# Kernel tuning notes

Measured on AMD Instinct MI355X. Metric: run time of the kernel, lower is better.

## Reference

```python
import jax, jax.numpy as jnp
import numpy as np

B = 128
J = 22
Q = J * 4          # 88
R = 3
C = 4
H = 512            # LSTM hidden
ENC = 256 * 3      # 768 concatenated encoder outputs
STATE_IN = Q + R + C   # 95
OFF_IN = Q + R         # 91
OUT = Q + R + C        # 95


def _linear_params(key, fan_in, fan_out):
    kw, kb = jax.random.split(key)
    s = 1.0 / np.sqrt(fan_in)
    w = jax.random.uniform(kw, (fan_in, fan_out), jnp.float32, -s, s)
    b = jax.random.uniform(kb, (fan_out,), jnp.float32, -s, s)
    return w, b


def setup_inputs() -> dict:
    key = jax.random.key(0)
    ks = jax.random.split(key, 24)
    inp = {
        "past_root_vel": jax.random.normal(ks[0], (B, 10, R)) * 0.1,
        "past_quats": jax.random.normal(ks[1], (B, 10, Q)),
        "past_root_offset": jax.random.normal(ks[2], (B, 10, R)),
        "past_quat_offset": jax.random.normal(ks[3], (B, 10, Q)),
        "past_contacts": jax.random.uniform(ks[4], (B, 10, C)),
        "target_root_pos": jax.random.normal(ks[5], (B, R)),
        "target_quats": jax.random.normal(ks[6], (B, Q)),
        "init_root_pos": jax.random.normal(ks[7], (B, R)),
        "pred_weights": jax.random.normal(ks[8], (B, 4 * H, ENC + H)) * 0.03,
        "pred_bias": jax.random.normal(ks[9], (B, 4 * H)) * 0.01,
    }
    inp["se_w1"], inp["se_b1"] = _linear_params(ks[10], STATE_IN, 512)
    inp["se_w2"], inp["se_b2"] = _linear_params(ks[11], 512, 256)
    inp["oe_w1"], inp["oe_b1"] = _linear_params(ks[12], OFF_IN, 512)
    inp["oe_w2"], inp["oe_b2"] = _linear_params(ks[13], 512, 256)
    inp["te_w1"], inp["te_b1"] = _linear_params(ks[14], Q, 512)
    inp["te_w2"], inp["te_b2"] = _linear_params(ks[15], 512, 256)
    inp["de_w1"], inp["de_b1"] = _linear_params(ks[16], H, 512)
    inp["de_w2"], inp["de_b2"] = _linear_params(ks[17], 512, 256)
    inp["de_w3"], inp["de_b3"] = _linear_params(ks[18], 256, OUT)
    return inp


def reference(past_root_vel, past_quats, past_root_offset, past_quat_offset,
              past_contacts, target_root_pos, target_quats, init_root_pos,
              pred_weights, pred_bias,
              se_w1, se_b1, se_w2, se_b2,
              oe_w1, oe_b1, oe_w2, oe_b2,
              te_w1, te_b1, te_w2, te_b2,
              de_w1, de_b1, de_w2, de_b2, de_w3, de_b3):
    b = past_quats.shape[0]

    def enc(x, w1, b1, w2, b2):
        return jax.nn.relu(jax.nn.relu(x @ w1 + b1) @ w2 + b2)

    # target encoding is identical every step; hoist it
    h_target = enc(target_quats, te_w1, te_b1, te_w2, te_b2)

    def step(root_vel, quats, root_offset, quat_offset, contacts, h, c):
        state_vec = jnp.concatenate([contacts, quats, root_vel], axis=1)
        offset_vec = jnp.concatenate([root_offset, quat_offset], axis=1)
        h_state = enc(state_vec, se_w1, se_b1, se_w2, se_b2)
        h_offset = enc(offset_vec, oe_w1, oe_b1, oe_w2, oe_b2)
        pred_in = jnp.concatenate([h_state, h_offset, h_target], axis=1)  # [B,768]
        # per-sample hypernetwork LSTM cell (torch gate order i,f,g,o)
        z = jnp.concatenate([pred_in, h], axis=1)  # [B, 1280]
        gates = jnp.einsum('boi,bi->bo', pred_weights, z) + pred_bias
        i_g, f_g, g_g, o_g = jnp.split(gates, 4, axis=1)
        c2 = jax.nn.sigmoid(f_g) * c + jax.nn.sigmoid(i_g) * jnp.tanh(g_g)
        h2 = jax.nn.sigmoid(o_g) * jnp.tanh(c2)
        # decoder (512,512,256,out), no activation on last layer
        d = jax.nn.relu(h2 @ de_w1 + de_b1)
        d = jax.nn.relu(d @ de_w2 + de_b2)
        out = d @ de_w3 + de_b3
        next_quats = out[:, :Q] + quats
        next_rvel = out[:, Q:Q + R] + root_vel
        next_contacts = jax.nn.sigmoid(out[:, Q + R:])
        nq = next_quats.reshape(b, Q // 4, 4)
        nq = nq / jnp.maximum(jnp.linalg.norm(nq, axis=2, keepdims=True), 1e-12)
        return next_rvel, nq.reshape(b, Q), next_contacts, h2, c2

    h0 = jnp.zeros((b, H), past_quats.dtype)
    c0 = jnp.zeros((b, H), past_quats.dtype)

    def past_body(carry, x):
        glob, h, c, _, _, _, _, _ = carry
        rvel, quats, roff, qoff, cont = x
        nrv, nq, nc, h2, c2 = step(rvel, quats, roff, qoff, cont, h, c)
        glob2 = glob + rvel
        nroff = glob2 - target_root_pos
        nqoff = nq - target_quats
        return (glob2, h2, c2, nrv, nq, nc, nroff, nqoff), None

    z3 = jnp.zeros((b, R), past_quats.dtype)
    init = (init_root_pos, h0, c0, z3,
            jnp.zeros((b, Q), past_quats.dtype),
            jnp.zeros((b, C), past_quats.dtype),
            z3, jnp.zeros((b, Q), past_quats.dtype))
    xs = (jnp.swapaxes(past_root_vel, 0, 1), jnp.swapaxes(past_quats, 0, 1),
          jnp.swapaxes(past_root_offset, 0, 1), jnp.swapaxes(past_quat_offset, 0, 1),
          jnp.swapaxes(past_contacts, 0, 1))
    carry, _ = jax.lax.scan(past_body, init, xs)
    glob, h, c, nrv, nq, nc, roff, qoff = carry

    first_frame = jnp.concatenate([nrv, nq], axis=1)  # NOTE: rvel not glob, as in source

    def trans_body(carry, _):
        glob, h, c, rvel, quats, cont, roff, qoff = carry
        nrv, nq, nc, h2, c2 = step(rvel, quats, roff, qoff, cont, h, c)
        glob2 = glob + nrv
        nroff = glob2 - target_root_pos
        nqoff = nq - target_quats
        pose = jnp.concatenate([glob2, nq], axis=1)
        return (glob2, h2, c2, nrv, nq, nc, nroff, nqoff), (pose, nc)

    carry2 = (glob, h, c, nrv, nq, nc, roff, qoff)
    _, (poses, conts) = jax.lax.scan(trans_body, carry2, None, length=29)

    pred_poses = jnp.concatenate([first_frame[:, None], jnp.swapaxes(poses, 0, 1)], axis=1)
    pred_contacts = jnp.concatenate([nc[:, None], jnp.swapaxes(conts, 0, 1)], axis=1)
    return pred_poses, pred_contacts
```

## Files before the change

### kernel.cpp

```cpp
#include <hip/hip_runtime.h>
#include <hip/hip_bf16.h>
#include <math.h>

#define BATCH 128
#define QD 88
#define HDIM 512
#define ZDIM 1280
#define GDIM 2048
#define PROW 1536
#define NPAST 10
#define NTRANS 29
#define NSTEPS (NPAST + NTRANS)
#define OUTD 95
#define POSE_ELEMS (BATCH * 30 * 91)

typedef float f32x4 __attribute__((ext_vector_type(4)));

__device__ __forceinline__ float sig_(float x) { return 1.0f / (1.0f + expf(-x)); }
__device__ __forceinline__ void dot4_(const uint4 wv, const float4 zv, float& d) {
    const float4 f = *(const float4*)&wv;
    d = fmaf(f.x, zv.x, d); d = fmaf(f.y, zv.y, d);
    d = fmaf(f.z, zv.z, d); d = fmaf(f.w, zv.w, d);
}
__device__ __forceinline__ void fma4_(float4& acc, float x, const float4 w) {
    acc.x = fmaf(x, w.x, acc.x); acc.y = fmaf(x, w.y, acc.y);
    acc.z = fmaf(x, w.z, acc.z); acc.w = fmaf(x, w.w, acc.w);
}
__device__ __forceinline__ unsigned q12_(float w, float inv) {
    const unsigned u = __float2uint_rn(fmaf(w, inv, 2048.0f));
    return (u > 4095u) ? 4095u : u;
}
__device__ __forceinline__ void pack12_(const uint4 a, const uint4 b, float inv,
                                        unsigned& o0, unsigned& o1, unsigned& o2) {
    const unsigned u0 = q12_(__uint_as_float(a.x), inv), u1 = q12_(__uint_as_float(a.y), inv);
    const unsigned u2 = q12_(__uint_as_float(a.z), inv), u3 = q12_(__uint_as_float(a.w), inv);
    const unsigned u4 = q12_(__uint_as_float(b.x), inv), u5 = q12_(__uint_as_float(b.y), inv);
    const unsigned u6 = q12_(__uint_as_float(b.z), inv), u7 = q12_(__uint_as_float(b.w), inv);
    o0 = u0 | (u1 << 12) | (u2 << 24);
    o1 = (u2 >> 8) | (u3 << 4) | (u4 << 16) | (u5 << 28);
    o2 = (u5 >> 4) | (u6 << 8) | (u7 << 20);
}
__device__ __forceinline__ float dot12_(unsigned d0, unsigned d1, unsigned d2,
                                        const float4 za, const float4 zb) {
    float acc = 0.f;
    acc = fmaf((float)((int)(d0 & 0xFFFu) - 2048), za.x, acc);
    acc = fmaf((float)((int)((d0 >> 12) & 0xFFFu) - 2048), za.y, acc);
    acc = fmaf((float)((int)((d0 >> 24) | ((d1 & 0xFu) << 8)) - 2048), za.z, acc);
    acc = fmaf((float)((int)((d1 >> 4) & 0xFFFu) - 2048), za.w, acc);
    acc = fmaf((float)((int)((d1 >> 16) & 0xFFFu) - 2048), zb.x, acc);
    acc = fmaf((float)((int)((d1 >> 28) | ((d2 & 0xFFu) << 4)) - 2048), zb.y, acc);
    acc = fmaf((float)((int)((d2 >> 8) & 0xFFFu) - 2048), zb.z, acc);
    acc = fmaf((float)((int)(d2 >> 20) - 2048), zb.w, acc);
    return acc;
}
__device__ __forceinline__ float wredmax_(float m) {
    #pragma unroll
    for (int s = 32; s >= 1; s >>= 1) m = fmaxf(m, __shfl_xor(m, s, 64));
    return m;
}
__device__ __forceinline__ float amax4_(const uint4 a, float m) {
    m = fmaxf(m, fabsf(__uint_as_float(a.x))); m = fmaxf(m, fabsf(__uint_as_float(a.y)));
    m = fmaxf(m, fabsf(__uint_as_float(a.z))); m = fmaxf(m, fabsf(__uint_as_float(a.w)));
    return m;
}

__global__ void __launch_bounds__(256)
matvec0_conv(const float* __restrict__ W, const float* __restrict__ z_ws,
             const float* __restrict__ pred_bias, unsigned char* __restrict__ Wp,
             float* __restrict__ scale_ws, float* __restrict__ g_ws, float* __restrict__ g0_ws)
{
    const int b = blockIdx.x >> 5, chunk = blockIdx.x & 31;
    const int wave = threadIdx.x >> 6, lane = threadIdx.x & 63;
    const int row0 = chunk * 64 + wave * 16;
    const float* zb = z_ws + b * ZDIM;
    const float biasv = (lane < 16) ? pred_bias[b * GDIM + row0 + lane] : 0.f;
    const int l4 = lane * 4;
    const float4 z0 = *(const float4*)(zb + l4);
    const float4 z1 = *(const float4*)(zb + 256 + l4);
    const float4 zh = *(const float4*)(zb + 512 + l4);
    const float4 z3 = *(const float4*)(zb + 768 + l4);
    const float4 z4 = *(const float4*)(zb + 1024 + l4);
    const char* wb = (const char*)W + (size_t)b * GDIM * ZDIM * 4;
    char* dstB = (char*)Wp + (size_t)b * GDIM * PROW;

    #define ISSUE(p, B) { const char* a_ = wb + (size_t)(row0 + 2 * (p)) * (ZDIM * 4) + lane * 16; \
        _Pragma("unroll") for (int i = 0; i < 10; ++i) B[i] = *(const uint4*)(a_ + i * 1024); }

    uint4 bufa[10], bufb[10];
    ISSUE(0, bufa);
    #pragma unroll
    for (int p = 0; p < 8; ++p) {
        uint4* cur = (p & 1) ? bufb : bufa;
        uint4* nxt = (p & 1) ? bufa : bufb;
        if (p < 7) ISSUE(p + 1, nxt);
        float dynA = 0.f, dynB = 0.f, statA = 0.f, statB = 0.f;
        dot4_(cur[0], z0, dynA); dot4_(cur[1], z1, dynA);
        dot4_(cur[2], zh, statA);
        dot4_(cur[3], z3, dynA); dot4_(cur[4], z4, dynA);
        dot4_(cur[5], z0, dynB); dot4_(cur[6], z1, dynB);
        dot4_(cur[7], zh, statB);
        dot4_(cur[8], z3, dynB); dot4_(cur[9], z4, dynB);
        float m0 = 0.f, m1 = 0.f;
        m0 = amax4_(cur[0], m0); m0 = amax4_(cur[1], m0);
        m0 = amax4_(cur[3], m0); m0 = amax4_(cur[4], m0);
        m1 = amax4_(cur[5], m1); m1 = amax4_(cur[6], m1);
        m1 = amax4_(cur[8], m1); m1 = amax4_(cur[9], m1);
        m0 = wredmax_(m0); m1 = wredmax_(m1);
        const float s0 = m0 * (1.f / 2047.f), s1 = m1 * (1.f / 2047.f);
        const float inv0 = (m0 > 0.f) ? 2047.f / m0 : 0.f;
        const float inv1 = (m1 > 0.f) ? 2047.f / m1 : 0.f;
        {
            char* rp = dstB + (size_t)(row0 + 2 * p) * PROW + lane * 12;
            unsigned o0, o1, o2;
            pack12_(cur[0], cur[1], inv0, o0, o1, o2);
            __builtin_nontemporal_store(o0, (unsigned*)(rp));
            __builtin_nontemporal_store(o1, (unsigned*)(rp + 4));
            __builtin_nontemporal_store(o2, (unsigned*)(rp + 8));
            pack12_(cur[3], cur[4], inv0, o0, o1, o2);
            __builtin_nontemporal_store(o0, (unsigned*)(rp + 768));
            __builtin_nontemporal_store(o1, (unsigned*)(rp + 772));
            __builtin_nontemporal_store(o2, (unsigned*)(rp + 776));
            pack12_(cur[5], cur[6], inv1, o0, o1, o2);
            __builtin_nontemporal_store(o0, (unsigned*)(rp + 1536));
            __builtin_nontemporal_store(o1, (unsigned*)(rp + 1540));
            __builtin_nontemporal_store(o2, (unsigned*)(rp + 1544));
            pack12_(cur[8], cur[9], inv1, o0, o1, o2);
            __builtin_nontemporal_store(o0, (unsigned*)(rp + 2304));
            __builtin_nontemporal_store(o1, (unsigned*)(rp + 2308));
            __builtin_nontemporal_store(o2, (unsigned*)(rp + 2312));
        }
        if (lane == 0) { scale_ws[b * GDIM + row0 + 2 * p] = s0;
                         scale_ws[b * GDIM + row0 + 2 * p + 1] = s1; }
        float sd0 = dynA + __shfl_xor(dynA, 32);
        float sd1 = dynB + __shfl_xor(dynB, 32);
        float ud = (lane < 32) ? sd0 : sd1;
        float ss0 = statA + __shfl_xor(statA, 32);
        float ss1 = statB + __shfl_xor(statB, 32);
        float us = (lane < 32) ? ss0 : ss1;
        #pragma unroll
        for (int m = 16; m >= 1; m >>= 1) { ud += __shfl_xor(ud, m); us += __shfl_xor(us, m); }
        const float badd = __shfl(biasv, 2 * p + ((lane >= 32) ? 1 : 0), 64);
        if (lane == 0 || lane == 32) {
            const int r = row0 + 2 * p + ((lane >= 32) ? 1 : 0);
            g0_ws[b * GDIM + r] = us + badd;
            g_ws[b * GDIM + r]  = ud + us + badd;
        }
    }
    #undef ISSUE
}

__global__ void __launch_bounds__(256)
epass(const unsigned char* __restrict__ Wp, const float* __restrict__ enc9,
      const float* __restrict__ scale_ws, const float* __restrict__ g0_ws,
      float* __restrict__ E_ws)
{
    const int b = blockIdx.x >> 5, chunk = blockIdx.x & 31;
    const int wave = threadIdx.x >> 6, lane = threadIdx.x & 63;
    const int row0 = chunk * 64 + wave * 16;
    const int l4 = lane * 4;
    float4 eA[9], eB[9];
    #pragma unroll
    for (int s = 0; s < 9; ++s) {
        const float* eb = enc9 + ((size_t)s * BATCH + b) * 512;
        eA[s] = *(const float4*)(eb + l4);
        eB[s] = *(const float4*)(eb + 256 + l4);
    }
    const float g0v = (lane < 16) ? g0_ws[b * GDIM + row0 + lane] : 0.f;
    const float scv = (lane < 16) ? scale_ws[b * GDIM + row0 + lane] : 0.f;
    const char* wb = (const char*)Wp + (size_t)b * GDIM * PROW;

    #define ISSUE(p, B) { const char* a_ = wb + (size_t)(row0 + 2 * (p)) * PROW + lane * 12; \
        B[0] = __builtin_nontemporal_load((const unsigned*)(a_)); \
        B[1] = __builtin_nontemporal_load((const unsigned*)(a_ + 4)); \
        B[2] = __builtin_nontemporal_load((const unsigned*)(a_ + 8)); \
        B[3] = __builtin_nontemporal_load((const unsigned*)(a_ + 1536)); \
        B[4] = __builtin_nontemporal_load((const unsigned*)(a_ + 1540)); \
        B[5] = __builtin_nontemporal_load((const unsigned*)(a_ + 1544)); }

    unsigned bufa[6], bufb[6];
    ISSUE(0, bufa);
    #pragma unroll
    for (int p = 0; p < 8; ++p) {
        unsigned* cur = (p & 1) ? bufb : bufa;
        unsigned* nxt = (p & 1) ? bufa : bufb;
        if (p < 7) ISSUE(p + 1, nxt);
        const float badd = __shfl(g0v, 2 * p + ((lane >= 32) ? 1 : 0), 64);
        const float srow = __shfl(scv, 2 * p + ((lane >= 32) ? 1 : 0), 64);
        #pragma unroll
        for (int s = 0; s < 9; ++s) {
            const float aA = dot12_(cur[0], cur[1], cur[2], eA[s], eB[s]);
            const float aB = dot12_(cur[3], cur[4], cur[5], eA[s], eB[s]);
            const float s0 = aA + __shfl_xor(aA, 32);
            const float s1 = aB + __shfl_xor(aB, 32);
            float u = (lane < 32) ? s0 : s1;
            #pragma unroll
            for (int m = 16; m >= 1; m >>= 1) u += __shfl_xor(u, m);
            const float val = badd + srow * u;
            if (lane == 0)
                E_ws[((size_t)s * BATCH + b) * GDIM + row0 + 2 * p] = val;
            else if (lane == 32)
                E_ws[((size_t)s * BATCH + b) * GDIM + row0 + 2 * p + 1] = val;
        }
    }
    #undef ISSUE
}

__global__ void __launch_bounds__(256)
matvecH(const unsigned char* __restrict__ Wp, const float* __restrict__ z_ws,
        const float* __restrict__ scale_ws, const float* __restrict__ Es,
        float* __restrict__ g_ws)
{
    const int b = blockIdx.x >> 5, chunk = blockIdx.x & 31;
    const int wave = threadIdx.x >> 6, lane = threadIdx.x & 63;
    const int row0 = chunk * 64 + wave * 16;
    const float* zb = z_ws + b * ZDIM;
    const int l4 = lane * 4;
    const float4 z3 = *(const float4*)(zb + 768 + l4);
    const float4 z4 = *(const float4*)(zb + 1024 + l4);
    const float Ev  = (lane < 16) ? Es[b * GDIM + row0 + lane] : 0.f;
    const float scv = (lane < 16) ? scale_ws[b * GDIM + row0 + lane] : 0.f;
    const char* wb = (const char*)Wp + (size_t)b * GDIM * PROW;

    #define ISSUE(p, B) { const char* a_ = wb + (size_t)(row0 + 2 * (p)) * PROW + 768 + lane * 12; \
        B[0] = *(const unsigned*)(a_);        B[1] = *(const unsigned*)(a_ + 4); \
        B[2] = *(const unsigned*)(a_ + 8); \
        B[3] = *(const unsigned*)(a_ + 1536); B[4] = *(const unsigned*)(a_ + 1540); \
        B[5] = *(const unsigned*)(a_ + 1544); }

    unsigned buf0[6], buf1[6], buf2[6];
    ISSUE(0, buf0);
    ISSUE(1, buf1);
    #pragma unroll
    for (int p = 0; p < 8; ++p) {
        unsigned* cur = (p % 3 == 0) ? buf0 : (p % 3 == 1) ? buf1 : buf2;
        unsigned* nxt = ((p + 2) % 3 == 0) ? buf0 : ((p + 2) % 3 == 1) ? buf1 : buf2;
        if (p < 6) ISSUE(p + 2, nxt);
        const float aA = dot12_(cur[0], cur[1], cur[2], z3, z4);
        const float aB = dot12_(cur[3], cur[4], cur[5], z3, z4);
        const float s0 = aA + __shfl_xor(aA, 32);
        const float s1 = aB + __shfl_xor(aB, 32);
        float u = (lane < 32) ? s0 : s1;
        #pragma unroll
        for (int m = 16; m >= 1; m >>= 1) u += __shfl_xor(u, m);
        const float badd = __shfl(Ev, 2 * p + ((lane >= 32) ? 1 : 0), 64);
        const float srow = __shfl(scv, 2 * p + ((lane >= 32) ? 1 : 0), 64);
        const float val = badd + srow * u;
        if (lane == 0)       g_ws[b * GDIM + row0 + 2 * p]     = val;
        else if (lane == 32) g_ws[b * GDIM + row0 + 2 * p + 1] = val;
    }
    #undef ISSUE
}

__global__ void __launch_bounds__(256)
matvec12(const unsigned char* __restrict__ Wp, const float* __restrict__ z_ws,
         const float* __restrict__ scale_ws, const float* __restrict__ g0_ws,
         float* __restrict__ g_ws)
{
    const int b = blockIdx.x >> 5, chunk = blockIdx.x & 31;
    const int wave = threadIdx.x >> 6, lane = threadIdx.x & 63;
    const int row0 = chunk * 64 + wave * 16;
    const float* zb = z_ws + b * ZDIM;
    const int l4 = lane * 4;
    const float4 z0 = *(const float4*)(zb + l4);
    const float4 z1 = *(const float4*)(zb + 256 + l4);
    const float4 z3 = *(const float4*)(zb + 768 + l4);
    const float4 z4 = *(const float4*)(zb + 1024 + l4);
    const float g0v = (lane < 16) ? g0_ws[b * GDIM + row0 + lane] : 0.f;
    const float scv = (lane < 16) ? scale_ws[b * GDIM + row0 + lane] : 0.f;
    const char* wb = (const char*)Wp + (size_t)b * GDIM * PROW;

    #define ISSUE(p, B) { const char* a_ = wb + (size_t)(row0 + 2 * (p)) * PROW + lane * 12; \
        B[0] = __builtin_nontemporal_load((const unsigned*)(a_)); \
        B[1] = __builtin_nontemporal_load((const unsigned*)(a_ + 4)); \
        B[2] = __builtin_nontemporal_load((const unsigned*)(a_ + 8)); \
        B[3] = __builtin_nontemporal_load((const unsigned*)(a_ + 768)); \
        B[4] = __builtin_nontemporal_load((const unsigned*)(a_ + 772)); \
        B[5] = __builtin_nontemporal_load((const unsigned*)(a_ + 776)); \
        B[6] = __builtin_nontemporal_load((const unsigned*)(a_ + 1536)); \
        B[7] = __builtin_nontemporal_load((const unsigned*)(a_ + 1540)); \
        B[8] = __builtin_nontemporal_load((const unsigned*)(a_ + 1544)); \
        B[9] = __builtin_nontemporal_load((const unsigned*)(a_ + 2304)); \
        B[10] = __builtin_nontemporal_load((const unsigned*)(a_ + 2308)); \
        B[11] = __builtin_nontemporal_load((const unsigned*)(a_ + 2312)); }

    unsigned buf0[12], buf1[12], buf2[12];
    ISSUE(0, buf0);
    ISSUE(1, buf1);
    #pragma unroll
    for (int p = 0; p < 8; ++p) {
        unsigned* cur = (p % 3 == 0) ? buf0 : (p % 3 == 1) ? buf1 : buf2;
        unsigned* nxt = ((p + 2) % 3 == 0) ? buf0 : ((p + 2) % 3 == 1) ? buf1 : buf2;
        if (p < 6) ISSUE(p + 2, nxt);
        const float aA = dot12_(cur[0], cur[1], cur[2], z0, z1)
                       + dot12_(cur[3], cur[4], cur[5], z3, z4);
        const float aB = dot12_(cur[6], cur[7], cur[8], z0, z1)
                       + dot12_(cur[9], cur[10], cur[11], z3, z4);
        const float s0 = aA + __shfl_xor(aA, 32);
        const float s1 = aB + __shfl_xor(aB, 32);
        float u = (lane < 32) ? s0 : s1;
        #pragma unroll
        for (int m = 16; m >= 1; m >>= 1) u += __shfl_xor(u, m);
        const float badd = __shfl(g0v, 2 * p + ((lane >= 32) ? 1 : 0), 64);
        const float srow = __shfl(scv, 2 * p + ((lane >= 32) ? 1 : 0), 64);
        const float val = badd + srow * u;
        if (lane == 0)       g_ws[b * GDIM + row0 + 2 * p]     = val;
        else if (lane == 32) g_ws[b * GDIM + row0 + 2 * p + 1] = val;
    }
    #undef ISSUE
}

__global__ void __launch_bounds__(512)
initk(const float* __restrict__ past_root_vel, const float* __restrict__ past_quats,
      const float* __restrict__ past_root_offset, const float* __restrict__ past_quat_offset,
      const float* __restrict__ past_contacts, const float* __restrict__ target_quats,
      const float* __restrict__ init_root_pos,
      const float* __restrict__ se_w1, const float* __restrict__ se_b1,
      const float* __restrict__ se_w2, const float* __restrict__ se_b2,
      const float* __restrict__ oe_w1, const float* __restrict__ oe_b1,
      const float* __restrict__ oe_w2, const float* __restrict__ oe_b2,
      const float* __restrict__ te_w1, const float* __restrict__ te_b1,
      const float* __restrict__ te_w2, const float* __restrict__ te_b2,
      float* __restrict__ z_ws, float* __restrict__ c_ws, float* __restrict__ car_ws)
{
    const int b = blockIdx.x, t = threadIdx.x;
    __shared__ float tq[QD], bufA[512], bufB[512], sv[95], ov[91];

    if (t < 192) car_ws[b * 192 + t] = (t < 3) ? init_root_pos[b * 3 + t] : 0.f;
    c_ws[b * HDIM + t] = 0.f;
    z_ws[b * ZDIM + 768 + t] = 0.f;
    if (t < QD) tq[t] = target_quats[b * QD + t];
    if (t < 4)  sv[t] = past_contacts[b * NPAST * 4 + t];
    if (t < QD) { sv[4 + t] = past_quats[b * NPAST * QD + t];
                  ov[3 + t] = past_quat_offset[b * NPAST * QD + t]; }
    if (t < 3)  { sv[92 + t] = past_root_vel[b * NPAST * 3 + t];
                  ov[t]      = past_root_offset[b * NPAST * 3 + t]; }
    __syncthreads();
    {
        float a = te_b1[t];
        #pragma unroll 8
        for (int i = 0; i < QD; ++i) a = fmaf(tq[i], te_w1[i * 512 + t], a);
        bufA[t] = fmaxf(a, 0.f);
    }
    __syncthreads();
    if (t < 256) {
        float a = te_b2[t];
        #pragma unroll 8
        for (int i = 0; i < 512; ++i) a = fmaf(bufA[i], te_w2[i * 256 + t], a);
        z_ws[b * ZDIM + 512 + t] = fmaxf(a, 0.f);
    }
    __syncthreads();
    {
        float aS = se_b1[t], aO = oe_b1[t];
        #pragma unroll 8
        for (int i = 0; i < 91; ++i) { aS = fmaf(sv[i], se_w1[i * 512 + t], aS);
                                       aO = fmaf(ov[i], oe_w1[i * 512 + t], aO); }
        #pragma unroll
        for (int i = 91; i < 95; ++i) aS = fmaf(sv[i], se_w1[i * 512 + t], aS);
        bufA[t] = fmaxf(aS, 0.f);
        bufB[t] = fmaxf(aO, 0.f);
    }
    __syncthreads();
    if (t < 256) {
        float a = se_b2[t];
        #pragma unroll 8
        for (int i = 0; i < 512; ++i) a = fmaf(bufA[i], se_w2[i * 256 + t], a);
        z_ws[b * ZDIM + t] = fmaxf(a, 0.f);
    } else {
        const int j = t - 256;
        float a = oe_b2[j];
        #pragma unroll 8
        for (int i = 0; i < 512; ++i) a = fmaf(bufB[i], oe_w2[i * 256 + j], a);
        z_ws[b * ZDIM + 256 + j] = fmaxf(a, 0.f);
    }
}

__global__ void __launch_bounds__(512)
enc_past(const float* __restrict__ past_root_vel, const float* __restrict__ past_quats,
         const float* __restrict__ past_root_offset, const float* __restrict__ past_quat_offset,
         const float* __restrict__ past_contacts,
         const float* __restrict__ se_w1, const float* __restrict__ se_b1,
         const float* __restrict__ se_w2, const float* __restrict__ se_b2,
         const float* __restrict__ oe_w1, const float* __restrict__ oe_b1,
         const float* __restrict__ oe_w2, const float* __restrict__ oe_b2,
         float* __restrict__ enc9)
{
    const int b = blockIdx.x, t = threadIdx.x;
    const int s = blockIdx.y + 1;
    __shared__ float bufA[512], bufB[512], sv[95], ov[91];

    if (t < 4)  sv[t] = past_contacts[(b * NPAST + s) * 4 + t];
    if (t < QD) { sv[4 + t] = past_quats[(b * NPAST + s) * QD + t];
                  ov[3 + t] = past_quat_offset[(b * NPAST + s) * QD + t]; }
    if (t < 3)  { sv[92 + t] = past_root_vel[(b * NPAST + s) * 3 + t];
                  ov[t]      = past_root_offset[(b * NPAST + s) * 3 + t]; }
    __syncthreads();
    {
        float aS = se_b1[t], aO = oe_b1[t];
        #pragma unroll 8
        for (int i = 0; i < 91; ++i) { aS = fmaf(sv[i], se_w1[i * 512 + t], aS);
                                       aO = fmaf(ov[i], oe_w1[i * 512 + t], aO); }
        #pragma unroll
        for (int i = 91; i < 95; ++i) aS = fmaf(sv[i], se_w1[i * 512 + t], aS);
        bufA[t] = fmaxf(aS, 0.f);
        bufB[t] = fmaxf(aO, 0.f);
    }
    __syncthreads();
    float* dst = enc9 + ((size_t)(s - 1) * BATCH + b) * 512;
    if (t < 256) {
        float a = se_b2[t];
        #pragma unroll 8
        for (int i = 0; i < 512; ++i) a = fmaf(bufA[i], se_w2[i * 256 + t], a);
        dst[t] = fmaxf(a, 0.f);
    } else {
        const int j = t - 256;
        float a = oe_b2[j];
        #pragma unroll 8
        for (int i = 0; i < 512; ++i) a = fmaf(bufB[i], oe_w2[i * 256 + j], a);
        dst[256 + j] = fmaxf(a, 0.f);
    }
}

__global__ void __launch_bounds__(512)
stepk(const float* __restrict__ past_root_vel, const float* __restrict__ past_quats,
      const float* __restrict__ past_root_offset, const float* __restrict__ past_quat_offset,
      const float* __restrict__ past_contacts, const float* __restrict__ target_root_pos,
      const float* __restrict__ target_quats,
      const float* __restrict__ se_w1, const float* __restrict__ se_b1,
      const float* __restrict__ se_w2, const float* __restrict__ se_b2,
      const float* __restrict__ oe_w1, const float* __restrict__ oe_b1,
      const float* __restrict__ oe_w2, const float* __restrict__ oe_b2,
      const float* __restrict__ de_w1, const float* __restrict__ de_b1,
      const float* __restrict__ de_w2, const float* __restrict__ de_b2,
      const float* __restrict__ de_w3, const float* __restrict__ de_b3,
      float* __restrict__ out, float* __restrict__ z_ws, const float* __restrict__ g_ws,
      float* __restrict__ c_ws, float* __restrict__ car_ws, int s, int skip_enc)
{
    const int b = blockIdx.x, t = threadIdx.x;
    __shared__ float4 part4[512];
    __shared__ __align__(16) float h2s[HDIM], bufA[512], bufB[512], d2[256];
    __shared__ float outv[OUTD], nq[QD], sv[95], ov[91], carryL[192], tq[QD], trp[3];
    __shared__ float rvn[3], globn[3], contn[4];

    if (t < 192) carryL[t] = car_ws[b * 192 + t];
    if (t < QD) tq[t] = target_quats[b * QD + t];
    if (t < 3)  trp[t] = target_root_pos[b * 3 + t];

    {
        const float* g = g_ws + b * GDIM;
        const float ig = g[t], fg = g[512 + t], gg = g[1024 + t], og = g[1536 + t];
        const float c2 = sig_(fg) * c_ws[b * HDIM + t] + sig_(ig) * tanhf(gg);
        c_ws[b * HDIM + t] = c2;
        const float h2 = sig_(og) * tanhf(c2);
        h2s[t] = h2;
        z_ws[b * ZDIM + 768 + t] = h2;
    }
    __syncthreads();
    {
        const int c = t & 127, s4 = t >> 7;
        float4 acc = {0.f, 0.f, 0.f, 0.f};
        const float* w = de_w1 + (size_t)(s4 * 128) * 512 + 4 * c;
        #pragma unroll 8
        for (int k = 0; k < 128; ++k)
            fma4_(acc, h2s[s4 * 128 + k], *(const float4*)(w + (size_t)k * 512));
        part4[t] = acc;
    }
    __syncthreads();
    if (t < 128) {
        float4 v = part4[t];
        #pragma unroll
        for (int s4 = 1; s4 < 4; ++s4) { const float4 p = part4[s4 * 128 + t];
            v.x += p.x; v.y += p.y; v.z += p.z; v.w += p.w; }
        const float4 bb = *(const float4*)(de_b1 + 4 * t);
        float4 r; r.x = fmaxf(v.x + bb.x, 0.f); r.y = fmaxf(v.y + bb.y, 0.f);
        r.z = fmaxf(v.z + bb.z, 0.f); r.w = fmaxf(v.w + bb.w, 0.f);
        *(float4*)&bufA[4 * t] = r;
    }
    __syncthreads();
    {
        const int c = t & 63, s8 = t >> 6;
        float4 acc = {0.f, 0.f, 0.f, 0.f};
        const float* w = de_w2 + (size_t)(s8 * 64) * 256 + 4 * c;
        #pragma unroll 8
        for (int k = 0; k < 64; ++k)
            fma4_(acc, bufA[s8 * 64 + k], *(const float4*)(w + (size_t)k * 256));
        part4[t] = acc;
    }
    __syncthreads();
    if (t < 64) {
        float4 v = part4[t];
        #pragma unroll
        for (int s8 = 1; s8 < 8; ++s8) { const float4 p = part4[s8 * 64 + t];
            v.x += p.x; v.y += p.y; v.z += p.z; v.w += p.w; }
        const float4 bb = *(const float4*)(de_b2 + 4 * t);
        float4 r; r.x = fmaxf(v.x + bb.x, 0.f); r.y = fmaxf(v.y + bb.y, 0.f);
        r.z = fmaxf(v.z + bb.z, 0.f); r.w = fmaxf(v.w + bb.w, 0.f);
        *(float4*)&d2[4 * t] = r;
    }
    __syncthreads();
    if (t < OUTD) {
        float acc = de_b3[t];
        #pragma unroll 16
        for (int i = 0; i < 256; ++i) acc = fmaf(d2[i], de_w3[i * OUTD + t], acc);
        outv[t] = acc;
    }
    __syncthreads();

    const bool pastS = (s < NPAST);
    if (t < QD) {
        const float qin = pastS ? past_quats[(b * NPAST + s) * QD + t] : carryL[10 + t];
        nq[t] = outv[t] + qin;
    }
    __syncthreads();
    if (t < 22) {
        const float a = nq[4 * t], b2 = nq[4 * t + 1], c3 = nq[4 * t + 2], d4 = nq[4 * t + 3];
        const float inv = 1.f / fmaxf(sqrtf(a * a + b2 * b2 + c3 * c3 + d4 * d4), 1e-12f);
        nq[4 * t] = a * inv; nq[4 * t + 1] = b2 * inv; nq[4 * t + 2] = c3 * inv; nq[4 * t + 3] = d4 * inv;
    }
    if (t < 3) {
        const float rin = pastS ? past_root_vel[(b * NPAST + s) * 3 + t] : carryL[3 + t];
        const float nrv = outv[88 + t] + rin;
        const float g = carryL[t] + (pastS ? rin : nrv);
        rvn[t] = nrv; globn[t] = g;
    }
    if (t < 4) contn[t] = sig_(outv[91 + t]);
    __syncthreads();

    if (t < 3) { car_ws[b * 192 + t] = globn[t]; car_ws[b * 192 + 3 + t] = rvn[t];
                 car_ws[b * 192 + 186 + t] = globn[t] - trp[t]; }
    if (t < 4) car_ws[b * 192 + 6 + t] = contn[t];
    if (t < QD) { car_ws[b * 192 + 10 + t] = nq[t]; car_ws[b * 192 + 98 + t] = nq[t] - tq[t]; }
    if (s == NPAST - 1) {
        const size_t pb = (size_t)b * 30 * 91;
        if (t < 3)  out[pb + t] = rvn[t];
        if (t < QD) out[pb + 3 + t] = nq[t];
        if (t < 4)  out[POSE_ELEMS + (size_t)b * 30 * 4 + t] = contn[t];
    } else if (!pastS) {
        const int k = s - NPAST + 1;
        const size_t pb = ((size_t)b * 30 + k) * 91;
        if (t < 3)  out[pb + t] = globn[t];
        if (t < QD) out[pb + 3 + t] = nq[t];
        if (t < 4)  out[POSE_ELEMS + ((size_t)b * 30 + k) * 4 + t] = contn[t];
    }
    if (s == NSTEPS - 1) return;
    if (skip_enc) return;

    const int nx = s + 1;
    if (nx < NPAST) {
        if (t < 4)  sv[t] = past_contacts[(b * NPAST + nx) * 4 + t];
        if (t < QD) { sv[4 + t] = past_quats[(b * NPAST + nx) * QD + t];
                      ov[3 + t] = past_quat_offset[(b * NPAST + nx) * QD + t]; }
        if (t < 3)  { sv[92 + t] = past_root_vel[(b * NPAST + nx) * 3 + t];
                      ov[t]      = past_root_offset[(b * NPAST + nx) * 3 + t]; }
    } else {
        if (t < 4)  sv[t] = contn[t];
        if (t < QD) { sv[4 + t] = nq[t]; ov[3 + t] = nq[t] - tq[t]; }
        if (t < 3)  { sv[92 + t] = rvn[t]; ov[t] = globn[t] - trp[t]; }
    }
    __syncthreads();
    {
        const int tt = t & 255, enc = t >> 8;
        const int c = tt & 127, sl = tt >> 7;
        const float* inp = enc ? ov : sv;
        const float* w1  = enc ? oe_w1 : se_w1;
        const int nin  = enc ? 91 : 95;
        const int half = enc ? 46 : 48;
        const int i0 = sl * half;
        const int iend = (i0 + half < nin) ? (i0 + half) : nin;
        float4 acc = {0.f, 0.f, 0.f, 0.f};
        #pragma unroll 8
        for (int k = 0; k < 48; ++k) {
            const int i = i0 + k;
            if (i < iend) fma4_(acc, inp[i], *(const float4*)(w1 + (size_t)i * 512 + 4 * c));
        }
        part4[enc * 256 + tt] = acc;
    }
    __syncthreads();
    if (t < 128) {
        const float4 a = part4[t], b2 = part4[128 + t];
        const float4 bb = *(const float4*)(se_b1 + 4 * t);
        float4 r; r.x = fmaxf(a.x + b2.x + bb.x, 0.f); r.y = fmaxf(a.y + b2.y + bb.y, 0.f);
        r.z = fmaxf(a.z + b2.z + bb.z, 0.f); r.w = fmaxf(a.w + b2.w + bb.w, 0.f);
        *(float4*)&bufA[4 * t] = r;
    } else if (t < 256) {
        const int c = t - 128;
        const float4 a = part4[256 + c], b2 = part4[384 + c];
        const float4 bb = *(const float4*)(oe_b1 + 4 * c);
        float4 r; r.x = fmaxf(a.x + b2.x + bb.x, 0.f); r.y = fmaxf(a.y + b2.y + bb.y, 0.f);
        r.z = fmaxf(a.z + b2.z + bb.z, 0.f); r.w = fmaxf(a.w + b2.w + bb.w, 0.f);
        *(float4*)&bufB[4 * c] = r;
    }
    __syncthreads();
    {
        const int tt = t & 255, enc = t >> 8;
        const int c = tt & 63, sl = tt >> 6;
        const float* inp = enc ? bufB : bufA;
        const float* w2  = enc ? oe_w2 : se_w2;
        float4 acc = {0.f, 0.f, 0.f, 0.f};
        const float* w = w2 + (size_t)(sl * 128) * 256 + 4 * c;
        #pragma unroll 8
        for (int k = 0; k < 128; ++k)
            fma4_(acc, inp[sl * 128 + k], *(const float4*)(w + (size_t)k * 256));
        part4[enc * 256 + tt] = acc;
    }
    __syncthreads();
    if (t < 64) {
        float4 v = part4[t];
        #pragma unroll
        for (int sl = 1; sl < 4; ++sl) { const float4 p = part4[sl * 64 + t];
            v.x += p.x; v.y += p.y; v.z += p.z; v.w += p.w; }
        const float4 bb = *(const float4*)(se_b2 + 4 * t);
        float4 r; r.x = fmaxf(v.x + bb.x, 0.f); r.y = fmaxf(v.y + bb.y, 0.f);
        r.z = fmaxf(v.z + bb.z, 0.f); r.w = fmaxf(v.w + bb.w, 0.f);
        *(float4*)(z_ws + b * ZDIM + 4 * t) = r;
    } else if (t < 128) {
        const int c = t - 64;
        float4 v = part4[256 + c];
        #pragma unroll
        for (int sl = 1; sl < 4; ++sl) { const float4 p = part4[256 + sl * 64 + c];
            v.x += p.x; v.y += p.y; v.z += p.z; v.w += p.w; }
        const float4 bb = *(const float4*)(oe_b2 + 4 * c);
        float4 r; r.x = fmaxf(v.x + bb.x, 0.f); r.y = fmaxf(v.y + bb.y, 0.f);
        r.z = fmaxf(v.z + bb.z, 0.f); r.w = fmaxf(v.w + bb.w, 0.f);
        *(float4*)(z_ws + b * ZDIM + 256 + 4 * c) = r;
    }
}

__global__ void __launch_bounds__(256)
matvec_f32(const float* __restrict__ W, const float* __restrict__ z_ws,
           const float* __restrict__ pred_bias, float* __restrict__ g_ws)
{
    const int b = blockIdx.x >> 5, chunk = blockIdx.x & 31;
    const int wave = threadIdx.x >> 6, lane = threadIdx.x & 63;
    const int row0 = chunk * 64 + wave * 16;
    const float* zb = z_ws + b * ZDIM;
    const float biasv = (lane < 16) ? pred_bias[b * GDIM + row0 + lane] : 0.f;
    const int l4 = lane * 4;
    const float4 z0 = *(const float4*)(zb + l4);
    const float4 z1 = *(const float4*)(zb + 256 + l4);
    const float4 z2 = *(const float4*)(zb + 512 + l4);
    const float4 z3 = *(const float4*)(zb + 768 + l4);
    const float4 z4 = *(const float4*)(zb + 1024 + l4);
    const char* wb = (const char*)W + (size_t)b * GDIM * ZDIM * 4;

    #define ISSUE(p, B) { const char* a_ = wb + (size_t)(row0 + 2 * (p)) * (ZDIM * 4) + lane * 16; \
        _Pragma("unroll") for (int i = 0; i < 10; ++i) B[i] = *(const uint4*)(a_ + i * 1024); }

    uint4 bufa[10], bufb[10];
    ISSUE(0, bufa);
    #pragma unroll
    for (int p = 0; p < 8; ++p) {
        uint4* cur = (p & 1) ? bufb : bufa;
        uint4* nxt = (p & 1) ? bufa : bufb;
        if (p < 7) ISSUE(p + 1, nxt);
        float accA = 0.f, accB = 0.f;
        dot4_(cur[0], z0, accA); dot4_(cur[1], z1, accA); dot4_(cur[2], z2, accA);
        dot4_(cur[3], z3, accA); dot4_(cur[4], z4, accA);
        dot4_(cur[5], z0, accB); dot4_(cur[6], z1, accB); dot4_(cur[7], z2, accB);
        dot4_(cur[8], z3, accB); dot4_(cur[9], z4, accB);
        float s0 = accA + __shfl_xor(accA, 32);
        float s1 = accB + __shfl_xor(accB, 32);
        float u = (lane < 32) ? s0 : s1;
        #pragma unroll
        for (int m = 16; m >= 1; m >>= 1) u += __shfl_xor(u, m);
        const float badd = __shfl(biasv, 2 * p + ((lane >= 32) ? 1 : 0), 64);
        if (lane == 0)       g_ws[b * GDIM + row0 + 2 * p]     = u + badd;
        else if (lane == 32) g_ws[b * GDIM + row0 + 2 * p + 1] = u + badd;
    }
    #undef ISSUE
}

extern "C" void kernel_launch(void* const* d_in, const int* in_sizes, int n_in,
                              void* d_out, int out_size, void* d_ws, size_t ws_size,
                              hipStream_t stream) {
    const float* prv = (const float*)d_in[0];
    const float* pq  = (const float*)d_in[1];
    const float* pro = (const float*)d_in[2];
    const float* pqo = (const float*)d_in[3];
    const float* pc  = (const float*)d_in[4];
    const float* trp = (const float*)d_in[5];
    const float* tq  = (const float*)d_in[6];
    const float* irp = (const float*)d_in[7];
    const float* pw  = (const float*)d_in[8];
    const float* pb  = (const float*)d_in[9];
    const float* se_w1 = (const float*)d_in[10]; const float* se_b1 = (const float*)d_in[11];
    const float* se_w2 = (const float*)d_in[12]; const float* se_b2 = (const float*)d_in[13];
    const float* oe_w1 = (const float*)d_in[14]; const float* oe_b1 = (const float*)d_in[15];
    const float* oe_w2 = (const float*)d_in[16]; const float* oe_b2 = (const float*)d_in[17];
    const float* te_w1 = (const float*)d_in[18]; const float* te_b1 = (const float*)d_in[19];
    const float* te_w2 = (const float*)d_in[20]; const float* te_b2 = (const float*)d_in[21];
    const float* de_w1 = (const float*)d_in[22]; const float* de_b1 = (const float*)d_in[23];
    const float* de_w2 = (const float*)d_in[24]; const float* de_b2 = (const float*)d_in[25];
    const float* de_w3 = (const float*)d_in[26]; const float* de_b3 = (const float*)d_in[27];
    float* outp = (float*)d_out;

    const size_t WPACKB = (size_t)BATCH * GDIM * PROW;
    const size_t AUXB = (size_t)BATCH * (GDIM * 3 + ZDIM + HDIM + 192) * 4
                      + (size_t)9 * BATCH * 512 * 4
                      + (size_t)9 * BATCH * GDIM * 4;
    const bool bf = ws_size >= WPACKB + AUXB;

    char* base = (char*)d_ws;
    float* scale_ws; float* g0_ws; float* z_ws;
    if (bf) {
        scale_ws = (float*)(base + WPACKB);
        g0_ws    = scale_ws + (size_t)BATCH * GDIM;
        z_ws     = g0_ws + (size_t)BATCH * GDIM;
    } else {
        scale_ws = nullptr;
        g0_ws    = nullptr;
        z_ws     = (float*)base;
    }
    float* g_ws    = z_ws + (size_t)BATCH * ZDIM;
    float* c_ws    = g_ws + (size_t)BATCH * GDIM;
    float* car_ws  = c_ws + (size_t)BATCH * HDIM;
    float* enc9_ws = car_ws + (size_t)BATCH * 192;
    float* E_ws    = enc9_ws + (size_t)9 * BATCH * 512;

    initk<<<dim3(BATCH), dim3(512), 0, stream>>>(prv, pq, pro, pqo, pc, tq, irp,
        se_w1, se_b1, se_w2, se_b2, oe_w1, oe_b1, oe_w2, oe_b2,
        te_w1, te_b1, te_w2, te_b2, z_ws, c_ws, car_ws);

    if (bf) {
        enc_past<<<dim3(BATCH, 9), dim3(512), 0, stream>>>(prv, pq, pro, pqo, pc,
            se_w1, se_b1, se_w2, se_b2, oe_w1, oe_b1, oe_w2, oe_b2, enc9_ws);
        matvec0_conv<<<dim3(BATCH * 32), dim3(256), 0, stream>>>(
            pw, z_ws, pb, (unsigned char*)d_ws, scale_ws, g_ws, g0_ws);
        epass<<<dim3(BATCH * 32), dim3(256), 0, stream>>>(
            (const unsigned char*)d_ws, enc9_ws, scale_ws, g0_ws, E_ws);
        for (int s = 0; s < NSTEPS; ++s) {
            if (s >= 1 && s < NPAST) {
                matvecH<<<dim3(BATCH * 32), dim3(256), 0, stream>>>(
                    (const unsigned char*)d_ws, z_ws, scale_ws,
                    E_ws + (size_t)(s - 1) * BATCH * GDIM, g_ws);
            } else if (s >= NPAST) {
                matvec12<<<dim3(BATCH * 32), dim3(256), 0, stream>>>(
                    (const unsigned char*)d_ws, z_ws, scale_ws, g0_ws, g_ws);
            }
            const int skip_enc = (s + 1 < NPAST) ? 1 : 0;
            stepk<<<dim3(BATCH), dim3(512), 0, stream>>>(prv, pq, pro, pqo, pc, trp, tq,
                se_w1, se_b1, se_w2, se_b2, oe_w1, oe_b1, oe_w2, oe_b2,
                de_w1, de_b1, de_w2, de_b2, de_w3, de_b3,
                outp, z_ws, g_ws, c_ws, car_ws, s, skip_enc);
        }
    } else {
        for (int s = 0; s < NSTEPS; ++s) {
            matvec_f32<<<dim3(BATCH * 32), dim3(256), 0, stream>>>(pw, z_ws, pb, g_ws);
            stepk<<<dim3(BATCH), dim3(512), 0, stream>>>(prv, pq, pro, pqo, pc, trp, tq,
                se_w1, se_b1, se_w2, se_b2, oe_w1, oe_b1, oe_w2, oe_b2,
                de_w1, de_b1, de_w2, de_b2, de_w3, de_b3,
                outp, z_ws, g_ws, c_ws, car_ws, s, 0);
        }
    }
}
```

Before: 4.232 ms.

## Interleave packed 12-bit weight rows in quads for 16-byte vector loads

Changes the packed 12-bit weight layout so that four rows are grouped into a 6144-byte quad block. Each lane then reads and writes 16-byte vectors instead of separate 4-byte words. The pack kernel buffers even-row outputs and emits six vector nontemporal stores per row pair, and all three consumer kernels (epass, the hidden-part gate kernel and the full gate kernel) switch to three or six u32x4 loads per quad. The aim is fewer, wider memory instructions on the bandwidth-bound weight streams, at the cost of more register state and a layout every reader must agree on.

```diff
diff --git a/kernel.cpp b/kernel.cpp
--- a/kernel.cpp
+++ b/kernel.cpp
@@ -8,6 +8,7 @@
 #define ZDIM 1280
 #define GDIM 2048
 #define PROW 1536
+#define QSTRIDE 6144
 #define NPAST 10
 #define NTRANS 29
 #define NSTEPS (NPAST + NTRANS)
@@ -15,6 +16,7 @@
 #define POSE_ELEMS (BATCH * 30 * 91)
 
 typedef float f32x4 __attribute__((ext_vector_type(4)));
+typedef unsigned int u32x4 __attribute__((ext_vector_type(4)));
 
 __device__ __forceinline__ float sig_(float x) { return 1.0f / (1.0f + expf(-x)); }
 __device__ __forceinline__ void dot4_(const uint4 wv, const float4 zv, float& d) {
@@ -87,6 +89,7 @@
         _Pragma("unroll") for (int i = 0; i < 10; ++i) B[i] = *(const uint4*)(a_ + i * 1024); }
 
     uint4 bufa[10], bufb[10];
+    unsigned sst[6], hst[6];
     ISSUE(0, bufa);
     #pragma unroll
     for (int p = 0; p < 8; ++p) {
@@ -109,25 +112,29 @@
         const float s0 = m0 * (1.f / 2047.f), s1 = m1 * (1.f / 2047.f);
         const float inv0 = (m0 > 0.f) ? 2047.f / m0 : 0.f;
         const float inv1 = (m1 > 0.f) ? 2047.f / m1 : 0.f;
-        {
-            char* rp = dstB + (size_t)(row0 + 2 * p) * PROW + lane * 12;
-            unsigned o0, o1, o2;
-            pack12_(cur[0], cur[1], inv0, o0, o1, o2);
-            __builtin_nontemporal_store(o0, (unsigned*)(rp));
-            __builtin_nontemporal_store(o1, (unsigned*)(rp + 4));
-            __builtin_nontemporal_store(o2, (unsigned*)(rp + 8));
-            pack12_(cur[3], cur[4], inv0, o0, o1, o2);
-            __builtin_nontemporal_store(o0, (unsigned*)(rp + 768));
-            __builtin_nontemporal_store(o1, (unsigned*)(rp + 772));
-            __builtin_nontemporal_store(o2, (unsigned*)(rp + 776));
-            pack12_(cur[5], cur[6], inv1, o0, o1, o2);
-            __builtin_nontemporal_store(o0, (unsigned*)(rp + 1536));
-            __builtin_nontemporal_store(o1, (unsigned*)(rp + 1540));
-            __builtin_nontemporal_store(o2, (unsigned*)(rp + 1544));
-            pack12_(cur[8], cur[9], inv1, o0, o1, o2);
-            __builtin_nontemporal_store(o0, (unsigned*)(rp + 2304));
-            __builtin_nontemporal_store(o1, (unsigned*)(rp + 2308));
-            __builtin_nontemporal_store(o2, (unsigned*)(rp + 2312));
+        unsigned s0a, s0b, s0c, h0a, h0b, h0c, s1a, s1b, s1c, h1a, h1b, h1c;
+        pack12_(cur[0], cur[1], inv0, s0a, s0b, s0c);
+        pack12_(cur[3], cur[4], inv0, h0a, h0b, h0c);
+        pack12_(cur[5], cur[6], inv1, s1a, s1b, s1c);
+        pack12_(cur[8], cur[9], inv1, h1a, h1b, h1c);
+        if ((p & 1) == 0) {
+            sst[0] = s0a; sst[1] = s0b; sst[2] = s0c; sst[3] = s1a; sst[4] = s1b; sst[5] = s1c;
+            hst[0] = h0a; hst[1] = h0b; hst[2] = h0c; hst[3] = h1a; hst[4] = h1b; hst[5] = h1c;
+        } else {
+            char* base = dstB + (size_t)((row0 + 2 * p) >> 2) * QSTRIDE + lane * 16;
+            u32x4 v;
+            v.x = sst[0]; v.y = sst[1]; v.z = sst[2]; v.w = sst[3];
+            __builtin_nontemporal_store(v, (u32x4*)(base));
+            v.x = sst[4]; v.y = sst[5]; v.z = s0a; v.w = s0b;
+            __builtin_nontemporal_store(v, (u32x4*)(base + 1024));
+            v.x = s0c; v.y = s1a; v.z = s1b; v.w = s1c;
+            __builtin_nontemporal_store(v, (u32x4*)(base + 2048));
+            v.x = hst[0]; v.y = hst[1]; v.z = hst[2]; v.w = hst[3];
+            __builtin_nontemporal_store(v, (u32x4*)(base + 3072));
+            v.x = hst[4]; v.y = hst[5]; v.z = h0a; v.w = h0b;
+            __builtin_nontemporal_store(v, (u32x4*)(base + 4096));
+            v.x = h0c; v.y = h1a; v.z = h1b; v.w = h1c;
+            __builtin_nontemporal_store(v, (u32x4*)(base + 5120));
         }
         if (lane == 0) { scale_ws[b * GDIM + row0 + 2 * p] = s0;
                          scale_ws[b * GDIM + row0 + 2 * p + 1] = s1; }
@@ -149,6 +156,22 @@
     #undef ISSUE
 }
 
+__device__ __forceinline__ void redwrite_(float rA, float rB, int lane,
+                                          float g0v, float scv, int idx0,
+                                          float* __restrict__ dst, int drow0) {
+    const float sA = rA + __shfl_xor(rA, 32);
+    const float sB = rB + __shfl_xor(rB, 32);
+    float u = (lane < 32) ? sA : sB;
+    #pragma unroll
+    for (int m = 16; m >= 1; m >>= 1) u += __shfl_xor(u, m);
+    const int hilo = (lane >= 32) ? 1 : 0;
+    const float badd = __shfl(g0v, idx0 + hilo, 64);
+    const float srow = __shfl(scv, idx0 + hilo, 64);
+    const float val = badd + srow * u;
+    if (lane == 0)       dst[drow0] = val;
+    else if (lane == 32) dst[drow0 + 1] = val;
+}
+
 __global__ void __launch_bounds__(256)
 epass(const unsigned char* __restrict__ Wp, const float* __restrict__ enc9,
       const float* __restrict__ scale_ws, const float* __restrict__ g0_ws,
@@ -157,6 +180,7 @@
     const int b = blockIdx.x >> 5, chunk = blockIdx.x & 31;
     const int wave = threadIdx.x >> 6, lane = threadIdx.x & 63;
     const int row0 = chunk * 64 + wave * 16;
+    const int q0 = row0 >> 2;
     const int l4 = lane * 4;
     float4 eA[9], eB[9];
     #pragma unroll
@@ -169,37 +193,27 @@
     const float scv = (lane < 16) ? scale_ws[b * GDIM + row0 + lane] : 0.f;
     const char* wb = (const char*)Wp + (size_t)b * GDIM * PROW;
 
-    #define ISSUE(p, B) { const char* a_ = wb + (size_t)(row0 + 2 * (p)) * PROW + lane * 12; \
-        B[0] = __builtin_nontemporal_load((const unsigned*)(a_)); \
-        B[1] = __builtin_nontemporal_load((const unsigned*)(a_ + 4)); \
-        B[2] = __builtin_nontemporal_load((const unsigned*)(a_ + 8)); \
-        B[3] = __builtin_nontemporal_load((const unsigned*)(a_ + 1536)); \
-        B[4] = __builtin_nontemporal_load((const unsigned*)(a_ + 1540)); \
-        B[5] = __builtin_nontemporal_load((const unsigned*)(a_ + 1544)); }
-
-    unsigned bufa[6], bufb[6];
+    #define ISSUE(qq, B) { const char* a_ = wb + (size_t)(q0 + (qq)) * QSTRIDE + lane * 16; \
+        B[0] = __builtin_nontemporal_load((const u32x4*)(a_)); \
+        B[1] = __builtin_nontemporal_load((const u32x4*)(a_ + 1024)); \
+        B[2] = __builtin_nontemporal_load((const u32x4*)(a_ + 2048)); }
+
+    u32x4 bufa[3], bufb[3];
     ISSUE(0, bufa);
     #pragma unroll
-    for (int p = 0; p < 8; ++p) {
-        unsigned* cur = (p & 1) ? bufb : bufa;
-        unsigned* nxt = (p & 1) ? bufa : bufb;
-        if (p < 7) ISSUE(p + 1, nxt);
-        const float badd = __shfl(g0v, 2 * p + ((lane >= 32) ? 1 : 0), 64);
-        const float srow = __shfl(scv, 2 * p + ((lane >= 32) ? 1 : 0), 64);
+    for (int qq = 0; qq < 4; ++qq) {
+        u32x4* cur = (qq & 1) ? bufb : bufa;
+        u32x4* nxt = (qq & 1) ? bufa : bufb;
+        if (qq < 3) ISSUE(qq + 1, nxt);
         #pragma unroll
         for (int s = 0; s < 9; ++s) {
-            const float aA = dot12_(cur[0], cur[1], cur[2], eA[s], eB[s]);
-            const float aB = dot12_(cur[3], cur[4], cur[5], eA[s], eB[s]);
-            const float s0 = aA + __shfl_xor(aA, 32);
-            const float s1 = aB + __shfl_xor(aB, 32);
-            float u = (lane < 32) ? s0 : s1;
-            #pragma unroll
-            for (int m = 16; m >= 1; m >>= 1) u += __shfl_xor(u, m);
-            const float val = badd + srow * u;
-            if (lane == 0)
-                E_ws[((size_t)s * BATCH + b) * GDIM + row0 + 2 * p] = val;
-            else if (lane == 32)
-                E_ws[((size_t)s * BATCH + b) * GDIM + row0 + 2 * p + 1] = val;
+            const float r0 = dot12_(cur[0].x, cur[0].y, cur[0].z, eA[s], eB[s]);
+            const float r1 = dot12_(cur[0].w, cur[1].x, cur[1].y, eA[s], eB[s]);
+            const float r2 = dot12_(cur[1].z, cur[1].w, cur[2].x, eA[s], eB[s]);
+            const float r3 = dot12_(cur[2].y, cur[2].z, cur[2].w, eA[s], eB[s]);
+            float* dst = E_ws + ((size_t)s * BATCH + b) * GDIM;
+            redwrite_(r0, r1, lane, g0v, scv, 4 * qq,     dst, row0 + 4 * qq);
+            redwrite_(r2, r3, lane, g0v, scv, 4 * qq + 2, dst, row0 + 4 * qq + 2);
         }
     }
     #undef ISSUE
@@ -213,6 +227,7 @@
     const int b = blockIdx.x >> 5, chunk = blockIdx.x & 31;
     const int wave = threadIdx.x >> 6, lane = threadIdx.x & 63;
     const int row0 = chunk * 64 + wave * 16;
+    const int q0 = row0 >> 2;
     const float* zb = z_ws + b * ZDIM;
     const int l4 = lane * 4;
     const float4 z3 = *(const float4*)(zb + 768 + l4);
@@ -221,32 +236,26 @@
     const float scv = (lane < 16) ? scale_ws[b * GDIM + row0 + lane] : 0.f;
     const char* wb = (const char*)Wp + (size_t)b * GDIM * PROW;
 
-    #define ISSUE(p, B) { const char* a_ = wb + (size_t)(row0 + 2 * (p)) * PROW + 768 + lane * 12; \
-        B[0] = *(const unsigned*)(a_);        B[1] = *(const unsigned*)(a_ + 4); \
-        B[2] = *(const unsigned*)(a_ + 8); \
-        B[3] = *(const unsigned*)(a_ + 1536); B[4] = *(const unsigned*)(a_ + 1540); \
-        B[5] = *(const unsigned*)(a_ + 1544); }
-
-    unsigned buf0[6], buf1[6], buf2[6];
+    #define ISSUE(qq, B) { const char* a_ = wb + (size_t)(q0 + (qq)) * QSTRIDE + 3072 + lane * 16; \
+        B[0] = *(const u32x4*)(a_); \
+        B[1] = *(const u32x4*)(a_ + 1024); \
+        B[2] = *(const u32x4*)(a_ + 2048); }
+
+    u32x4 buf0[3], buf1[3], buf2[3];
     ISSUE(0, buf0);
     ISSUE(1, buf1);
     #pragma unroll
-    for (int p = 0; p < 8; ++p) {
-        unsigned* cur = (p % 3 == 0) ? buf0 : (p % 3 == 1) ? buf1 : buf2;
-        unsigned* nxt = ((p + 2) % 3 == 0) ? buf0 : ((p + 2) % 3 == 1) ? buf1 : buf2;
-        if (p < 6) ISSUE(p + 2, nxt);
-        const float aA = dot12_(cur[0], cur[1], cur[2], z3, z4);
-        const float aB = dot12_(cur[3], cur[4], cur[5], z3, z4);
-        const float s0 = aA + __shfl_xor(aA, 32);
-        const float s1 = aB + __shfl_xor(aB, 32);
-        float u = (lane < 32) ? s0 : s1;
-        #pragma unroll
-        for (int m = 16; m >= 1; m >>= 1) u += __shfl_xor(u, m);
-        const float badd = __shfl(Ev, 2 * p + ((lane >= 32) ? 1 : 0), 64);
-        const float srow = __shfl(scv, 2 * p + ((lane >= 32) ? 1 : 0), 64);
-        const float val = badd + srow * u;
-        if (lane == 0)       g_ws[b * GDIM + row0 + 2 * p]     = val;
-        else if (lane == 32) g_ws[b * GDIM + row0 + 2 * p + 1] = val;
+    for (int qq = 0; qq < 4; ++qq) {
+        u32x4* cur = (qq % 3 == 0) ? buf0 : (qq % 3 == 1) ? buf1 : buf2;
+        u32x4* nxt = ((qq + 2) % 3 == 0) ? buf0 : ((qq + 2) % 3 == 1) ? buf1 : buf2;
+        if (qq < 2) ISSUE(qq + 2, nxt);
+        const float r0 = dot12_(cur[0].x, cur[0].y, cur[0].z, z3, z4);
+        const float r1 = dot12_(cur[0].w, cur[1].x, cur[1].y, z3, z4);
+        const float r2 = dot12_(cur[1].z, cur[1].w, cur[2].x, z3, z4);
+        const float r3 = dot12_(cur[2].y, cur[2].z, cur[2].w, z3, z4);
+        float* dst = g_ws + b * GDIM;
+        redwrite_(r0, r1, lane, Ev, scv, 4 * qq,     dst, row0 + 4 * qq);
+        redwrite_(r2, r3, lane, Ev, scv, 4 * qq + 2, dst, row0 + 4 * qq + 2);
     }
     #undef ISSUE
 }
@@ -259,6 +268,7 @@
     const int b = blockIdx.x >> 5, chunk = blockIdx.x & 31;
     const int wave = threadIdx.x >> 6, lane = threadIdx.x & 63;
     const int row0 = chunk * 64 + wave * 16;
+    const int q0 = row0 >> 2;
     const float* zb = z_ws + b * ZDIM;
     const int l4 = lane * 4;
     const float4 z0 = *(const float4*)(zb + l4);
@@ -269,42 +279,33 @@
     const float scv = (lane < 16) ? scale_ws[b * GDIM + row0 + lane] : 0.f;
     const char* wb = (const char*)Wp + (size_t)b * GDIM * PROW;
 
-    #define ISSUE(p, B) { const char* a_ = wb + (size_t)(row0 + 2 * (p)) * PROW + lane * 12; \
-        B[0] = __builtin_nontemporal_load((const unsigned*)(a_)); \
-        B[1] = __builtin_nontemporal_load((const unsigned*)(a_ + 4)); \
-        B[2] = __builtin_nontemporal_load((const unsigned*)(a_ + 8)); \
-        B[3] = __builtin_nontemporal_load((const unsigned*)(a_ + 768)); \
-        B[4] = __builtin_nontemporal_load((const unsigned*)(a_ + 772)); \
-        B[5] = __builtin_nontemporal_load((const unsigned*)(a_ + 776)); \
-        B[6] = __builtin_nontemporal_load((const unsigned*)(a_ + 1536)); \
-        B[7] = __builtin_nontemporal_load((const unsigned*)(a_ + 1540)); \
-        B[8] = __builtin_nontemporal_load((const unsigned*)(a_ + 1544)); \
-        B[9] = __builtin_nontemporal_load((const unsigned*)(a_ + 2304)); \
-        B[10] = __builtin_nontemporal_load((const unsigned*)(a_ + 2308)); \
-        B[11] = __builtin_nontemporal_load((const unsigned*)(a_ + 2312)); }
-
-    unsigned buf0[12], buf1[12], buf2[12];
+    #define ISSUE(qq, B) { const char* a_ = wb + (size_t)(q0 + (qq)) * QSTRIDE + lane * 16; \
+        B[0] = __builtin_nontemporal_load((const u32x4*)(a_)); \
+        B[1] = __builtin_nontemporal_load((const u32x4*)(a_ + 1024)); \
+        B[2] = __builtin_nontemporal_load((const u32x4*)(a_ + 2048)); \
+        B[3] = __builtin_nontemporal_load((const u32x4*)(a_ + 3072)); \
+        B[4] = __builtin_nontemporal_load((const u32x4*)(a_ + 4096)); \
+        B[5] = __builtin_nontemporal_load((const u32x4*)(a_ + 5120)); }
+
+    u32x4 buf0[6], buf1[6], buf2[6];
     ISSUE(0, buf0);
     ISSUE(1, buf1);
     #pragma unroll
-    for (int p = 0; p < 8; ++p) {
-        unsigned* cur = (p % 3 == 0) ? buf0 : (p % 3 == 1) ? buf1 : buf2;
-        unsigned* nxt = ((p + 2) % 3 == 0) ? buf0 : ((p + 2) % 3 == 1) ? buf1 : buf2;
-        if (p < 6) ISSUE(p + 2, nxt);
-        const float aA = dot12_(cur[0], cur[1], cur[2], z0, z1)
-                       + dot12_(cur[3], cur[4], cur[5], z3, z4);
-        const float aB = dot12_(cur[6], cur[7], cur[8], z0, z1)
-                       + dot12_(cur[9], cur[10], cur[11], z3, z4);
-        const float s0 = aA + __shfl_xor(aA, 32);
-        const float s1 = aB + __shfl_xor(aB, 32);
-        float u = (lane < 32) ? s0 : s1;
-        #pragma unroll
-        for (int m = 16; m >= 1; m >>= 1) u += __shfl_xor(u, m);
-        const float badd = __shfl(g0v, 2 * p + ((lane >= 32) ? 1 : 0), 64);
-        const float srow = __shfl(scv, 2 * p + ((lane >= 32) ? 1 : 0), 64);
-        const float val = badd + srow * u;
-        if (lane == 0)       g_ws[b * GDIM + row0 + 2 * p]     = val;
-        else if (lane == 32) g_ws[b * GDIM + row0 + 2 * p + 1] = val;
+    for (int qq = 0; qq < 4; ++qq) {
+        u32x4* cur = (qq % 3 == 0) ? buf0 : (qq % 3 == 1) ? buf1 : buf2;
+        u32x4* nxt = ((qq + 2) % 3 == 0) ? buf0 : ((qq + 2) % 3 == 1) ? buf1 : buf2;
+        if (qq < 2) ISSUE(qq + 2, nxt);
+        const float r0 = dot12_(cur[0].x, cur[0].y, cur[0].z, z0, z1)
+                       + dot12_(cur[3].x, cur[3].y, cur[3].z, z3, z4);
+        const float r1 = dot12_(cur[0].w, cur[1].x, cur[1].y, z0, z1)
+                       + dot12_(cur[3].w, cur[4].x, cur[4].y, z3, z4);
+        const float r2 = dot12_(cur[1].z, cur[1].w, cur[2].x, z0, z1)
+                       + dot12_(cur[4].z, cur[4].w, cur[5].x, z3, z4);
+        const float r3 = dot12_(cur[2].y, cur[2].z, cur[2].w, z0, z1)
+                       + dot12_(cur[5].y, cur[5].z, cur[5].w, z3, z4);
+        float* dst = g_ws + b * GDIM;
+        redwrite_(r0, r1, lane, g0v, scv, 4 * qq,     dst, row0 + 4 * qq);
+        redwrite_(r2, r3, lane, g0v, scv, 4 * qq + 2, dst, row0 + 4 * qq + 2);
     }
     #undef ISSUE
 }
```

Measured after the change: 4.261 ms. No clear change (+0.7%).
